# Kernel tuning notes

Measured on AMD Instinct MI355X. Metric: run time of the kernel, lower is better.

Reference implementation:

```python
import math
import jax, jax.numpy as jnp
import numpy as np

B, S, HID = 1, 2048, 2048
NH, QLR, KVLR = 16, 1536, 512
QKD, QKP, VD = 128, 64, 128          # nope dim, rope dim, v dim
IH, ID, TOPK = 4, 128, 512            # indexer heads, indexer head dim, topk
EPS = 1e-6
NEG = -1e9
_MS = 0.1 * 1.0 * math.log(40.0) + 1.0           # mscale adjustment, rope_factor=40
SCALE = _MS * _MS / math.sqrt(QKD + QKP)          # main attention softmax scale
IDX_SCALE = ID ** -0.5                            # indexer softmax scale


def _freqs_cos_sin():
    # seqlen <= original_max_position_embeddings -> plain RoPE freqs (no YaRN branch)
    freqs = 1.0 / (10000.0 ** (jnp.arange(0, QKP, 2, dtype=jnp.float32) / QKP))  # [QKP/2]
    ang = jnp.outer(jnp.arange(S, dtype=jnp.float32), freqs)                      # [S, QKP/2]
    return jnp.cos(ang)[None, :, None, :], jnp.sin(ang)[None, :, None, :]         # [1,S,1,QKP/2]


def _rope_interleaved(x, cos, sin):
    # pairs are (x[..., 2i], x[..., 2i+1])
    x1, x2 = x[..., 0::2], x[..., 1::2]
    yr = x1 * cos - x2 * sin
    yi = x1 * sin + x2 * cos
    return jnp.stack([yr, yi], axis=-1).reshape(x.shape)


def _rope_half(x, cos, sin):
    # interleaved=False: real = first half, imag = second half; output [reals..., imags...]
    d2 = x.shape[-1] // 2
    x1, x2 = x[..., :d2], x[..., d2:]
    return jnp.concatenate([x1 * cos - x2 * sin, x1 * sin + x2 * cos], axis=-1)


def _rmsnorm(x, w):
    return x * jax.lax.rsqrt(jnp.mean(x * x, axis=-1, keepdims=True) + EPS) * w


def _layernorm(x, w, b):
    m = jnp.mean(x, axis=-1, keepdims=True)
    v = jnp.mean((x - m) ** 2, axis=-1, keepdims=True)
    return (x - m) * jax.lax.rsqrt(v + EPS) * w + b


def _indexer(x, qr, cos, sin, mask3, idx_wq_b, idx_wk, idx_kn_w, idx_kn_b, idx_ww):
    # x, qr detached by caller. mask3: [B,S,S]
    q = (qr @ idx_wq_b.T).reshape(B, S, IH, ID)
    q_pe, q_nope = q[..., :QKP], q[..., QKP:]
    q_pe = _rope_half(q_pe, cos, sin)
    q = jnp.concatenate([q_pe, q_nope], axis=-1)                   # [B,S,IH,ID]
    k = _layernorm(x @ idx_wk.T, idx_kn_w, idx_kn_b)               # [B,S,ID]
    k_pe, k_nope = k[..., :QKP], k[..., QKP:]
    k_pe = _rope_half(k_pe[:, :, None, :], cos, sin)[:, :, 0, :]
    k = jnp.concatenate([k_pe, k_nope], axis=-1)                   # [B,S,ID]
    weights = (x @ idx_ww.T) * (IH ** -0.5)                        # [B,S,IH]
    logits = jnp.einsum('bthd,bsd->bths', q, k) * IDX_SCALE        # [B,T,IH,S]
    logits = jax.nn.relu(logits)
    logits = jnp.einsum('bths,bth->bts', logits, weights)          # weighted head sum
    logits = logits + mask3
    topk_vals, topk_idx = jax.lax.top_k(logits, TOPK)
    log_topk_prob = jax.nn.log_softmax(topk_vals, axis=-1)
    return topk_idx, log_topk_prob


def reference(hidden_states, attention_mask, wq_down, q_ln_w, wq_up, wkv_down,
              kv_ln_w, wk_up, wv_up, wo, idx_wq_b, idx_wk, idx_kn_w, idx_kn_b, idx_ww):
    x = jnp.swapaxes(hidden_states, 0, 1)                          # [B,S,HID]
    mask3 = attention_mask[:, 0]                                   # [B,S,S]
    cos, sin = _freqs_cos_sin()

    qr = _rmsnorm(x @ wq_down.T, q_ln_w)                           # [B,S,QLR]
    q = (qr @ wq_up.T).reshape(B, S, NH, QKD + QKP)
    q_nope, q_pe = q[..., :QKD], q[..., QKD:]
    q_pe = _rope_interleaved(q_pe, cos, sin)

    kv = x @ wkv_down.T                                            # [B,S,KVLR+QKP]
    kv_c, k_pe = kv[..., :KVLR], kv[..., KVLR:]
    kv_c = _rmsnorm(kv_c, kv_ln_w)
    k_pe = _rope_interleaved(k_pe[:, :, None, :], cos, sin)        # [B,S,1,QKP]

    k_up_w = wk_up.reshape(NH, QKD, KVLR)
    q_abs = jnp.einsum('bshd,hdc->bshc', q_nope, k_up_w)           # absorbed q
    q_abs = jnp.concatenate([q_abs, q_pe], axis=-1)                # [B,S,NH,KVLR+QKP]

    topk_idx, log_topk_prob = _indexer(
        jax.lax.stop_gradient(x), jax.lax.stop_gradient(qr), cos, sin, mask3,
        idx_wq_b, idx_wk, idx_kn_w, idx_kn_b, idx_ww)

    keys = jnp.concatenate([kv_c, k_pe[:, :, 0, :]], axis=-1)      # [B,T,KVLR+QKP]
    scores = jnp.einsum('bshd,btd->bsht', q_abs, keys) * SCALE     # [B,S,NH,T]
    scores = scores + mask3[:, :, None, :]
    bi = jnp.arange(B)[:, None, None]
    si = jnp.arange(S)[None, :, None]
    index_mask = jnp.full((B, S, S), NEG, jnp.float32).at[bi, si, topk_idx].set(0.0)
    scores = scores + index_mask[:, :, None, :]
    probs = jax.nn.softmax(scores, axis=-1)                        # [B,S,NH,T]
    attn_out = jnp.einsum('bsht,btd->bshd', probs, kv_c)           # values = kv_c

    idx4 = jnp.broadcast_to(topk_idx[:, :, None, :], (B, S, NH, TOPK))
    sparse_probs = jnp.take_along_axis(jax.lax.stop_gradient(probs), idx4, axis=-1)
    attn_score = sparse_probs.sum(axis=2)
    attn_score = attn_score / attn_score.sum(axis=-1, keepdims=True)
    tgt = jnp.clip(jnp.log(attn_score), -100.0, 0.0)
    inp = jnp.clip(log_topk_prob, -100.0, 0.0)
    kl = jnp.sum(jnp.exp(tgt) * (tgt - inp))

    v_up_w = wv_up.reshape(NH, VD, KVLR)
    attn_out = jnp.einsum('bshc,hdc->bshd', attn_out, v_up_w)
    out = attn_out.reshape(B, S, NH * VD) @ wo.T
    return jnp.swapaxes(out, 0, 1), kl


def setup_inputs():
    key = jax.random.key(0)
    ks = jax.random.split(key, 12)
    p = lambda k, sh: jax.random.normal(k, sh, jnp.float32) * 0.02
    hidden_states = jax.random.normal(ks[0], (S, B, HID), jnp.float32)
    causal = jnp.where(jnp.arange(S)[:, None] >= jnp.arange(S)[None, :], 0.0, NEG).astype(jnp.float32)
    attention_mask = jnp.broadcast_to(causal, (B, 1, S, S))
    return dict(
        hidden_states=hidden_states,
        attention_mask=attention_mask,
        wq_down=p(ks[1], (QLR, HID)),
        q_ln_w=jnp.ones((QLR,), jnp.float32),
        wq_up=p(ks[2], (NH * (QKD + QKP), QLR)),
        wkv_down=p(ks[3], (KVLR + QKP, HID)),
        kv_ln_w=jnp.ones((KVLR,), jnp.float32),
        wk_up=p(ks[4], (NH * QKD, KVLR)),
        wv_up=p(ks[5], (NH * VD, KVLR)),
        wo=p(ks[6], (HID, NH * VD)),
        idx_wq_b=p(ks[7], (IH * ID, QLR)),
        idx_wk=p(ks[8], (ID, HID)),
        idx_kn_w=jnp.ones((ID,), jnp.float32),
        idx_kn_b=jnp.zeros((ID,), jnp.float32),
        idx_ww=p(ks[9], (IH, HID)),
    )
```

## Files before the change

kernel.cpp:

```cpp
#include <hip/hip_runtime.h>
#include <hip/hip_bf16.h>
#include <math.h>

typedef __hip_bfloat16 bf16;
typedef __attribute__((ext_vector_type(8))) short short8v;
typedef __attribute__((ext_vector_type(4))) float f32x4;

static constexpr float EPS_   = 1e-6f;
static constexpr float NEG_   = -1000000000.0f;
static constexpr float SCALE_ = 0.13523378f;
static constexpr float IDXSC_ = 0.08838834764832f;
static constexpr double LN10K_32 = 0.28782313662425575;

#define MFMA16(a, b, c) __builtin_amdgcn_mfma_f32_16x16x32_bf16(a, b, c, 0, 0, 0)

__device__ __forceinline__ void gld16(const void* g, void* l) {
  __builtin_amdgcn_global_load_lds(
      (const __attribute__((address_space(1))) void*)g,
      (__attribute__((address_space(3))) void*)l, 16, 0, 0);
}

static __device__ float block_reduce_op(float v, int op) {
  __shared__ float red_s[16];
  int lane = threadIdx.x & 63, wid = threadIdx.x >> 6;
  #pragma unroll
  for (int off = 32; off > 0; off >>= 1) {
    float o = __shfl_down(v, off);
    v = op ? fmaxf(v, o) : (v + o);
  }
  __syncthreads();
  if (lane == 0) red_s[wid] = v;
  __syncthreads();
  if (threadIdx.x == 0) {
    int nw = ((int)blockDim.x + 63) >> 6;
    float r = red_s[0];
    for (int i = 1; i < nw; i++) r = op ? fmaxf(r, red_s[i]) : (r + red_s[i]);
    red_s[0] = r;
  }
  __syncthreads();
  return red_s[0];
}

__global__ __launch_bounds__(256) void f2b_kernel(const float* __restrict__ in,
                                                  bf16* __restrict__ out, long n) {
  long i = ((long)blockIdx.x * 256 + threadIdx.x) * 4;
  if (i + 3 < n) {
    float4 v = *(const float4*)(in + i);
    out[i] = __float2bfloat16(v.x); out[i+1] = __float2bfloat16(v.y);
    out[i+2] = __float2bfloat16(v.z); out[i+3] = __float2bfloat16(v.w);
  } else {
    for (int j = 0; j < 4 && i + j < n; j++) out[i+j] = __float2bfloat16(in[i+j]);
  }
}

template <int BT, int OB>
__global__ __launch_bounds__(256) void gemm_bf16(
    const bf16* __restrict__ A, const bf16* __restrict__ B, void* __restrict__ Cv,
    int M, int N, int K, int lda, int ldb, int ldc, long sA, long sB, long sC) {
  A += (long)blockIdx.z * sA;
  B += (long)blockIdx.z * sB;
  __shared__ bf16 As[4096];
  __shared__ bf16 Bs[4096];
  const int m0 = blockIdx.y * 128, n0 = blockIdx.x * 128;
  const int tid = threadIdx.x;
  const int wave = tid >> 6, lane = tid & 63, g = lane >> 4, li = lane & 15;
  const int mB = (wave >> 1) * 64, nB = (wave & 1) * 64;
  f32x4 acc[4][4];
  #pragma unroll
  for (int i = 0; i < 4; i++)
    #pragma unroll
    for (int j = 0; j < 4; j++) acc[i][j] = (f32x4){0.f, 0.f, 0.f, 0.f};

  for (int k0 = 0; k0 < K; k0 += 32) {
    #pragma unroll
    for (int r2 = 0; r2 < 2; r2++) {
      int idx = r2 * 256 + tid;
      int row = idx >> 2, ko = (idx & 3) * 8;
      gld16(A + (long)(m0 + row) * lda + k0 + ko, &As[idx * 8]);
    }
    if (BT) {
      #pragma unroll
      for (int r2 = 0; r2 < 2; r2++) {
        int idx = r2 * 256 + tid;
        int row = idx >> 2, ko = (idx & 3) * 8;
        int rr = n0 + row; if (rr >= N) rr = N - 1;
        gld16(B + (long)rr * ldb + k0 + ko, &Bs[idx * 8]);
      }
    } else {
      int k = tid >> 3, nb = (tid & 7) * 16;
      const bf16* src = B + (long)(k0 + k) * ldb + n0 + nb;
      short8v v0 = *(const short8v*)src;
      short8v v1 = *(const short8v*)(src + 8);
      #pragma unroll
      for (int j = 0; j < 8; j++) {
        Bs[(nb + j) * 32 + k]     = ((const bf16*)&v0)[j];
        Bs[(nb + 8 + j) * 32 + k] = ((const bf16*)&v1)[j];
      }
    }
    __syncthreads();
    short8v af[4], bfr[4];
    #pragma unroll
    for (int mt = 0; mt < 4; mt++) af[mt]  = *(const short8v*)&As[(mB + mt*16 + li) * 32 + g*8];
    #pragma unroll
    for (int nt = 0; nt < 4; nt++) bfr[nt] = *(const short8v*)&Bs[(nB + nt*16 + li) * 32 + g*8];
    #pragma unroll
    for (int mt = 0; mt < 4; mt++)
      #pragma unroll
      for (int nt = 0; nt < 4; nt++)
        acc[mt][nt] = MFMA16(af[mt], bfr[nt], acc[mt][nt]);
    __syncthreads();
  }
  #pragma unroll
  for (int mt = 0; mt < 4; mt++)
    #pragma unroll
    for (int nt = 0; nt < 4; nt++)
      #pragma unroll
      for (int r = 0; r < 4; r++) {
        int row = m0 + mB + mt*16 + g*4 + r;
        int col = n0 + nB + nt*16 + li;
        if (col < N) {
          long off = (long)blockIdx.z * sC + (long)row * ldc + col;
          if (OB) ((bf16*)Cv)[off] = __float2bfloat16(acc[mt][nt][r]);
          else    ((float*)Cv)[off] = acc[mt][nt][r];
        }
      }
}

__global__ __launch_bounds__(256) void rmsnorm_b_kernel(const float* __restrict__ x,
                                                        const float* __restrict__ w,
                                                        bf16* __restrict__ out, int D) {
  const float* r = x + (long)blockIdx.x * D;
  bf16* o = out + (long)blockIdx.x * D;
  float ss = 0.f;
  for (int i = threadIdx.x; i < D; i += 256) { float v = r[i]; ss = fmaf(v, v, ss); }
  ss = block_reduce_op(ss, 0);
  float sc = rsqrtf(ss / (float)D + EPS_);
  for (int i = threadIdx.x; i < D; i += 256) o[i] = __float2bfloat16(r[i] * sc * w[i]);
}

__global__ __launch_bounds__(256) void kv_norm_rope_kernel(const float* __restrict__ kv,
                                                           const float* __restrict__ w,
                                                           bf16* __restrict__ keys_b) {
  int s = blockIdx.x;
  const float* r = kv + (long)s * 576;
  float ss = 0.f;
  for (int i = threadIdx.x; i < 512; i += 256) { float v = r[i]; ss = fmaf(v, v, ss); }
  ss = block_reduce_op(ss, 0);
  float sc = rsqrtf(ss / 512.f + EPS_);
  for (int i = threadIdx.x; i < 512; i += 256)
    keys_b[(long)s * 576 + i] = __float2bfloat16(r[i] * sc * w[i]);
  if (threadIdx.x < 32) {
    int j = threadIdx.x;
    float f = (float)exp(-(double)j * LN10K_32);
    float ang = (float)s * f;
    float c = cosf(ang), sn = sinf(ang);
    float x1 = r[512 + 2*j], x2 = r[512 + 2*j + 1];
    keys_b[(long)s * 576 + 512 + 2*j]     = __float2bfloat16(x1 * c - x2 * sn);
    keys_b[(long)s * 576 + 512 + 2*j + 1] = __float2bfloat16(x1 * sn + x2 * c);
  }
}

__global__ __launch_bounds__(256) void rope_q_kernel(const bf16* __restrict__ q,
                                                     bf16* __restrict__ qabs) {
  int idx = blockIdx.x * 256 + threadIdx.x;
  int j = idx & 31, h = (idx >> 5) & 15, s = idx >> 9;
  float f = (float)exp(-(double)j * LN10K_32);
  float ang = (float)s * f;
  float c = cosf(ang), sn = sinf(ang);
  const bf16* src = q + (long)s * 3072 + h * 192 + 128;
  float x1 = __bfloat162float(src[2*j]), x2 = __bfloat162float(src[2*j+1]);
  bf16* dst = qabs + (long)s * 9216 + h * 576 + 512;
  dst[2*j]     = __float2bfloat16(x1 * c - x2 * sn);
  dst[2*j + 1] = __float2bfloat16(x1 * sn + x2 * c);
}

__global__ __launch_bounds__(256) void rope_qi_kernel(bf16* __restrict__ qi) {
  int idx = blockIdx.x * 256 + threadIdx.x;
  int j = idx & 31, ih = (idx >> 5) & 3, s = idx >> 7;
  float f = (float)exp(-(double)j * LN10K_32);
  float ang = (float)s * f;
  float c = cosf(ang), sn = sinf(ang);
  bf16* p = qi + (long)s * 512 + ih * 128;
  float x1 = __bfloat162float(p[j]), x2 = __bfloat162float(p[32 + j]);
  p[j]      = __float2bfloat16(x1 * c - x2 * sn);
  p[32 + j] = __float2bfloat16(x1 * sn + x2 * c);
}

__global__ __launch_bounds__(128) void ki_ln_rope_kernel(const float* __restrict__ kt,
                                                         const float* __restrict__ w,
                                                         const float* __restrict__ b,
                                                         bf16* __restrict__ ki_b) {
  int s = blockIdx.x, d = threadIdx.x;
  float v = kt[(long)s * 128 + d];
  float m = block_reduce_op(v, 0) * (1.f / 128.f);
  float dv = v - m;
  float var = block_reduce_op(dv * dv, 0) * (1.f / 128.f);
  float y = dv * rsqrtf(var + EPS_) * w[d] + b[d];
  __shared__ float ys[128];
  ys[d] = y;
  __syncthreads();
  float out;
  if (d < 64) {
    int j = d & 31;
    float f = (float)exp(-(double)j * LN10K_32);
    float ang = (float)s * f;
    float c = cosf(ang), sn = sinf(ang);
    float x1 = ys[j], x2 = ys[32 + j];
    out = (d < 32) ? (x1 * c - x2 * sn) : (x1 * sn + x2 * c);
  } else out = y;
  ki_b[(long)s * 128 + d] = __float2bfloat16(out);
}

__global__ __launch_bounds__(256) void wgt_kernel(const float* __restrict__ x,
                                                  const float* __restrict__ ww,
                                                  float* __restrict__ wgt) {
  int s = blockIdx.x;
  float a0 = 0, a1 = 0, a2 = 0, a3 = 0;
  for (int i = threadIdx.x; i < 2048; i += 256) {
    float xv = x[(long)s * 2048 + i];
    a0 = fmaf(xv, ww[i], a0);
    a1 = fmaf(xv, ww[2048 + i], a1);
    a2 = fmaf(xv, ww[4096 + i], a2);
    a3 = fmaf(xv, ww[6144 + i], a3);
  }
  a0 = block_reduce_op(a0, 0);
  a1 = block_reduce_op(a1, 0);
  a2 = block_reduce_op(a2, 0);
  a3 = block_reduce_op(a3, 0);
  if (threadIdx.x == 0) {
    wgt[s*4+0] = 0.5f*a0; wgt[s*4+1] = 0.5f*a1; wgt[s*4+2] = 0.5f*a2; wgt[s*4+3] = 0.5f*a3;
  }
}

__global__ __launch_bounds__(256) void idx_logits_mfma(const bf16* __restrict__ qi,
                                                       const bf16* __restrict__ ki,
                                                       const float* __restrict__ wgt,
                                                       float* __restrict__ logits) {
  const int t0 = blockIdx.y * 64, s0 = blockIdx.x * 128;
  const int tid = threadIdx.x, wave = tid >> 6, lane = tid & 63;
  const int g = lane >> 4, li = lane & 15;
  if (s0 > t0 + 63) {
    #pragma unroll
    for (int j = 0; j < 8; j++)
      #pragma unroll
      for (int r = 0; r < 4; r++) {
        int t = t0 + wave*16 + g*4 + r, sidx = s0 + j*16 + li;
        logits[(long)t * 2048 + sidx] = NEG_;
      }
    return;
  }
  f32x4 acc[8];
  #pragma unroll
  for (int j = 0; j < 8; j++) acc[j] = (f32x4){0.f,0.f,0.f,0.f};
  #pragma unroll
  for (int h = 0; h < 4; h++) {
    f32x4 tmp[8];
    #pragma unroll
    for (int j = 0; j < 8; j++) tmp[j] = (f32x4){0.f,0.f,0.f,0.f};
    const bf16* arow = qi + ((long)(t0 + wave*16 + li) * 4 + h) * 128 + g*8;
    #pragma unroll
    for (int ks = 0; ks < 4; ks++) {
      short8v a = *(const short8v*)(arow + ks*32);
      #pragma unroll
      for (int j = 0; j < 8; j++) {
        const bf16* brow = ki + (long)(s0 + j*16 + li) * 128 + ks*32 + g*8;
        tmp[j] = MFMA16(a, *(const short8v*)brow, tmp[j]);
      }
    }
    #pragma unroll
    for (int r = 0; r < 4; r++) {
      float wv = wgt[(t0 + wave*16 + g*4 + r)*4 + h];
      #pragma unroll
      for (int j = 0; j < 8; j++)
        acc[j][r] += fmaxf(tmp[j][r] * IDXSC_, 0.f) * wv;
    }
  }
  #pragma unroll
  for (int j = 0; j < 8; j++)
    #pragma unroll
    for (int r = 0; r < 4; r++) {
      int t = t0 + wave*16 + g*4 + r, sidx = s0 + j*16 + li;
      logits[(long)t * 2048 + sidx] = acc[j][r] + (sidx <= t ? 0.f : NEG_);
    }
}

__global__ __launch_bounds__(256) void topk_kernel(const float* __restrict__ logits,
                                                   int* __restrict__ tki,
                                                   float* __restrict__ tkv,
                                                   float* __restrict__ logZ) {
  int t = blockIdx.x;
  __shared__ unsigned skeys[2048];
  __shared__ unsigned hist[256];
  __shared__ float svals[512];
  __shared__ int s_want;
  __shared__ unsigned s_prefix;
  const float* row = logits + (long)t * 2048;
  for (int i = threadIdx.x; i < 2048; i += 256) {
    unsigned u = __float_as_uint(row[i]);
    skeys[i] = (u & 0x80000000u) ? ~u : (u | 0x80000000u);
  }
  if (threadIdx.x == 0) { s_want = 512; s_prefix = 0u; }
  __syncthreads();
  for (int shift = 24; shift >= 0; shift -= 8) {
    if (threadIdx.x < 256) hist[threadIdx.x] = 0u;
    __syncthreads();
    unsigned pmask = (shift == 24) ? 0u : (0xFFFFFFFFu << (shift + 8));
    unsigned pref = s_prefix;
    for (int i = threadIdx.x; i < 2048; i += 256) {
      unsigned k = skeys[i];
      if ((k & pmask) == pref) atomicAdd(&hist[(k >> shift) & 255u], 1u);
    }
    __syncthreads();
    if (threadIdx.x == 0) {
      int want = s_want;
      unsigned cum = 0;
      int b = 255;
      for (;; b--) {
        cum += hist[b];
        if ((int)cum >= want || b == 0) break;
      }
      s_want = want - (int)(cum - hist[b]);
      s_prefix = pref | ((unsigned)b << shift);
    }
    __syncthreads();
  }
  unsigned T = s_prefix;
  int want_eq = s_want;
  int c_gt = 512 - want_eq;
  if (threadIdx.x < 64) {
    int n_gt = 0, n_eq = 0;
    unsigned long long below = (1ull << threadIdx.x) - 1ull;
    for (int base = 0; base < 2048; base += 64) {
      int i = base + (int)threadIdx.x;
      unsigned k = skeys[i];
      bool gt = (k > T), eq = (k == T);
      unsigned long long bg = __ballot(gt);
      unsigned long long be = __ballot(eq);
      int slot = -1;
      if (gt) slot = n_gt + (int)__popcll(bg & below);
      else if (eq) {
        int er = n_eq + (int)__popcll(be & below);
        if (er < want_eq) slot = c_gt + er;
      }
      if (slot >= 0) {
        unsigned bits = (k & 0x80000000u) ? (k ^ 0x80000000u) : ~k;
        float val = __uint_as_float(bits);
        tki[(long)t * 512 + slot] = i;
        tkv[(long)t * 512 + slot] = val;
        svals[slot] = val;
      }
      n_gt += (int)__popcll(bg);
      n_eq += (int)__popcll(be);
    }
  }
  __syncthreads();
  float m = -3.4e38f;
  for (int i = threadIdx.x; i < 512; i += 256) m = fmaxf(m, svals[i]);
  m = block_reduce_op(m, 1);
  float se = 0.f;
  for (int i = threadIdx.x; i < 512; i += 256) se += expf(svals[i] - m);
  se = block_reduce_op(se, 0);
  if (threadIdx.x == 0) logZ[t] = m + logf(se);
}

__global__ __launch_bounds__(256, 6) void attn_qk(
    const bf16* __restrict__ qabs, const bf16* __restrict__ keys,
    const int* __restrict__ tki, const float* __restrict__ tkv,
    const float* __restrict__ logZ, bf16* __restrict__ Pg,
    float* __restrict__ kl) {
  const int s = 2047 - blockIdx.x;
  const int tid = threadIdx.x;
  const int wave = tid >> 6, lane = tid & 63, g = lane >> 4, li = lane & 15;
  __shared__ int idxs[512];
  __shared__ __align__(16) bf16 ph[16 * 512];
  __shared__ float red[64];
  __shared__ float mxf[16], dnf[16];

  for (int i = tid; i < 512; i += 256) idxs[i] = tki[(long)s * 512 + i];
  __syncthreads();

  const bf16* qrow = qabs + (long)s * 9216 + li * 576 + g * 8;
  f32x4 accS[8];
  int kid[8];
  const bf16* kr[8];
  #pragma unroll
  for (int j = 0; j < 8; j++) {
    accS[j] = (f32x4){0.f,0.f,0.f,0.f};
    kid[j] = idxs[(wave * 8 + j) * 16 + li];
    kr[j] = keys + (long)kid[j] * 576 + g * 8;
  }
  short8v af = *(const short8v*)qrow;
  short8v kf[8];
  #pragma unroll
  for (int j = 0; j < 8; j++) kf[j] = *(const short8v*)kr[j];
  for (int ks = 0; ks < 18; ks++) {
    const int nko = (ks < 17 ? ks + 1 : 17) * 32;
    short8v afn = *(const short8v*)(qrow + nko);
    short8v nx[8];
    #pragma unroll
    for (int j = 0; j < 8; j++) nx[j] = *(const short8v*)(kr[j] + nko);
    #pragma unroll
    for (int j = 0; j < 8; j++) accS[j] = MFMA16(af, kf[j], accS[j]);
    af = afn;
    #pragma unroll
    for (int j = 0; j < 8; j++) kf[j] = nx[j];
  }

  float e[8][4];
  float m4[4];
  #pragma unroll
  for (int r = 0; r < 4; r++) m4[r] = -3.4e38f;
  #pragma unroll
  for (int j = 0; j < 8; j++) {
    float mask = (kid[j] <= s) ? 0.f : NEG_;
    #pragma unroll
    for (int r = 0; r < 4; r++) {
      e[j][r] = accS[j][r] * SCALE_ + mask;
      m4[r] = fmaxf(m4[r], e[j][r]);
    }
  }
  #pragma unroll
  for (int d = 1; d < 16; d <<= 1)
    #pragma unroll
    for (int r = 0; r < 4; r++) m4[r] = fmaxf(m4[r], __shfl_xor(m4[r], d));
  if (li == 0)
    #pragma unroll
    for (int r = 0; r < 4; r++) red[wave * 16 + g * 4 + r] = m4[r];
  __syncthreads();
  if (tid < 16) mxf[tid] = fmaxf(fmaxf(red[tid], red[16 + tid]), fmaxf(red[32 + tid], red[48 + tid]));
  __syncthreads();
  float d4[4] = {0.f, 0.f, 0.f, 0.f};
  #pragma unroll
  for (int j = 0; j < 8; j++)
    #pragma unroll
    for (int r = 0; r < 4; r++) {
      e[j][r] = __expf(e[j][r] - mxf[g * 4 + r]);
      d4[r] += e[j][r];
    }
  #pragma unroll
  for (int d = 1; d < 16; d <<= 1)
    #pragma unroll
    for (int r = 0; r < 4; r++) d4[r] += __shfl_xor(d4[r], d);
  if (li == 0)
    #pragma unroll
    for (int r = 0; r < 4; r++) red[wave * 16 + g * 4 + r] = d4[r];
  __syncthreads();
  if (tid < 16) dnf[tid] = red[tid] + red[16 + tid] + red[32 + tid] + red[48 + tid];
  __syncthreads();

  float invd[4];
  #pragma unroll
  for (int r = 0; r < 4; r++) invd[r] = 1.f / dnf[g * 4 + r];

  float tasj[8];
  #pragma unroll
  for (int j = 0; j < 8; j++) {
    float t = 0.f;
    #pragma unroll
    for (int r = 0; r < 4; r++) t += e[j][r] * invd[r];
    t += __shfl_xor(t, 16);
    t += __shfl_xor(t, 32);
    tasj[j] = t;
  }
  float klacc = 0.f;
  if (g == 0) {
    float lz = logZ[s];
    #pragma unroll
    for (int j = 0; j < 8; j++) {
      int slot = (wave * 8 + j) * 16 + li;
      float tgt = fminf(fmaxf(logf(tasj[j] * 0.0625f), -100.f), 0.f);
      float inp = fminf(fmaxf(tkv[(long)s * 512 + slot] - lz, -100.f), 0.f);
      klacc += expf(tgt) * (tgt - inp);
    }
  }
  #pragma unroll
  for (int d = 1; d < 16; d <<= 1) klacc += __shfl_xor(klacc, d);
  if (lane == 0) atomicAdd(kl, klacc);

  const int m = s >> 7;
  const int Km = (m + 1) << 7;
  const int rr = s & 127;
  bf16* Pbase = Pg + 131072L * m * (m + 1);
  for (int base = 0; base < Km; base += 512) {
    const int cw = min(512, Km - base);
    __syncthreads();
    { uint4 z = {0,0,0,0};
      for (int i = tid; i < 1024; i += 256) ((uint4*)ph)[i] = z; }
    __syncthreads();
    #pragma unroll
    for (int j = 0; j < 8; j++) {
      int kk = kid[j] - base;
      if (0 <= kk && kk < 512) {
        #pragma unroll
        for (int r = 0; r < 4; r++)
          ph[(g * 4 + r) * 512 + kk] = __float2bfloat16(e[j][r] * invd[r]);
      }
    }
    __syncthreads();
    for (int u = tid; u < 1024; u += 256) {
      int h = u >> 6, c = (u & 63) * 8;
      if (c < cw)
        *(short8v*)(Pbase + ((long)(h * 128 + rr) * Km + base + c)) =
            *(const short8v*)&ph[h * 512 + c];
    }
  }
}

__global__ __launch_bounds__(256) void attn_pv(const bf16* __restrict__ Pg,
                                               const bf16* __restrict__ keys,
                                               bf16* __restrict__ aoc) {
  const int m = 15 - blockIdx.y;
  const int h = blockIdx.z;
  const int Km = (m + 1) << 7;
  const bf16* A = Pg + 131072L * m * (m + 1) + (long)h * 128 * Km;
  const int n0 = blockIdx.x * 128;
  __shared__ bf16 As[4096];
  __shared__ bf16 Bs[4096];
  const int tid = threadIdx.x;
  const int wave = tid >> 6, lane = tid & 63, g = lane >> 4, li = lane & 15;
  const int mB = (wave >> 1) * 64, nB = (wave & 1) * 64;
  f32x4 acc[4][4];
  #pragma unroll
  for (int i = 0; i < 4; i++)
    #pragma unroll
    for (int j = 0; j < 4; j++) acc[i][j] = (f32x4){0.f, 0.f, 0.f, 0.f};

  for (int k0 = 0; k0 < Km; k0 += 32) {
    #pragma unroll
    for (int r2 = 0; r2 < 2; r2++) {
      int idx = r2 * 256 + tid;
      int row = idx >> 2, ko = (idx & 3) * 8;
      gld16(A + (long)row * Km + k0 + ko, &As[idx * 8]);
    }
    {
      int k = tid >> 3, nb = (tid & 7) * 16;
      const bf16* src = keys + (long)(k0 + k) * 576 + n0 + nb;
      short8v v0 = *(const short8v*)src;
      short8v v1 = *(const short8v*)(src + 8);
      #pragma unroll
      for (int j = 0; j < 8; j++) {
        Bs[(nb + j) * 32 + k]     = ((const bf16*)&v0)[j];
        Bs[(nb + 8 + j) * 32 + k] = ((const bf16*)&v1)[j];
      }
    }
    __syncthreads();
    short8v af[4], bfr[4];
    #pragma unroll
    for (int mt = 0; mt < 4; mt++) af[mt]  = *(const short8v*)&As[(mB + mt*16 + li) * 32 + g*8];
    #pragma unroll
    for (int nt = 0; nt < 4; nt++) bfr[nt] = *(const short8v*)&Bs[(nB + nt*16 + li) * 32 + g*8];
    #pragma unroll
    for (int mt = 0; mt < 4; mt++)
      #pragma unroll
      for (int nt = 0; nt < 4; nt++)
        acc[mt][nt] = MFMA16(af[mt], bfr[nt], acc[mt][nt]);
    __syncthreads();
  }
  #pragma unroll
  for (int mt = 0; mt < 4; mt++)
    #pragma unroll
    for (int nt = 0; nt < 4; nt++)
      #pragma unroll
      for (int r = 0; r < 4; r++) {
        int row = m * 128 + mB + mt*16 + g*4 + r;
        int col = n0 + nB + nt*16 + li;
        aoc[(long)row * 8192 + h * 512 + col] = __float2bfloat16(acc[mt][nt][r]);
      }
}

__global__ void zero_kernel(float* p) {
  if (threadIdx.x == 0 && blockIdx.x == 0) p[0] = 0.f;
}
__global__ void copykl_kernel(const float* src, float* dst) { dst[0] = src[0]; }

extern "C" void kernel_launch(void* const* d_in, const int* in_sizes, int n_in,
                              void* d_out, int out_size, void* d_ws, size_t ws_size,
                              hipStream_t stream) {
  (void)in_sizes; (void)n_in; (void)out_size; (void)ws_size;
  const float* x        = (const float*)d_in[0];
  const float* wq_down  = (const float*)d_in[2];
  const float* q_ln_w   = (const float*)d_in[3];
  const float* wq_up    = (const float*)d_in[4];
  const float* wkv_down = (const float*)d_in[5];
  const float* kv_ln_w  = (const float*)d_in[6];
  const float* wk_up    = (const float*)d_in[7];
  const float* wv_up    = (const float*)d_in[8];
  const float* wo       = (const float*)d_in[9];
  const float* idx_wq_b = (const float*)d_in[10];
  const float* idx_wk   = (const float*)d_in[11];
  const float* idx_kn_w = (const float*)d_in[12];
  const float* idx_kn_b = (const float*)d_in[13];
  const float* idx_ww   = (const float*)d_in[14];
  float* out = (float*)d_out;

  char* w = (char*)d_ws;
  size_t off = 0;
  auto alloc = [&](size_t bytes) { void* p = w + off; off += (bytes + 255) & ~255ul; return p; };
  bf16* keys_b  = (bf16*)alloc(2048L*576*2);
  bf16* qabs_b  = (bf16*)alloc(2048L*9216*2);
  bf16* aoc_b   = (bf16*)alloc(2048L*8192*2);
  bf16* ao_b    = (bf16*)alloc(2048L*2048*2);
  bf16* wvu_b   = (bf16*)alloc(16L*128*512*2);
  bf16* wo_b    = (bf16*)alloc(2048L*2048*2);
  float* tkv    = (float*)alloc(2048L*512*4);
  float* logZ   = (float*)alloc(2048*4);
  float* klbuf  = (float*)alloc(64);
  int*   tki    = (int*)alloc(2048L*512*4);
  size_t scratch0 = off;
  bf16* Pg = (bf16*)(w + scratch0);
  float* qr     = (float*)alloc(2048L*1536*4);
  float* kvtmp  = (float*)alloc(2048L*576*4);
  float* kitmp  = (float*)alloc(2048L*128*4);
  float* logits = (float*)alloc(2048L*2048*4);
  float* wgt    = (float*)alloc(2048L*4*4);
  bf16* x_b     = (bf16*)alloc(2048L*2048*2);
  bf16* qr_b    = (bf16*)alloc(2048L*1536*2);
  bf16* q_b     = (bf16*)alloc(2048L*3072*2);
  bf16* qi_b    = (bf16*)alloc(2048L*512*2);
  bf16* ki_b    = (bf16*)alloc(2048L*128*2);
  bf16* wqd_b   = (bf16*)alloc(1536L*2048*2);
  bf16* wqu_b   = (bf16*)alloc(3072L*1536*2);
  bf16* wkv_b   = (bf16*)alloc(576L*2048*2);
  bf16* wku_b   = (bf16*)alloc(16L*128*512*2);
  bf16* iwq_b   = (bf16*)alloc(512L*1536*2);
  bf16* iwk_b   = (bf16*)alloc(128L*2048*2);
  size_t pg_end = scratch0 + 131072ul*16*17*2;
  if (off < pg_end) off = pg_end;

  dim3 b256(256);
  auto cvt = [&](const float* src, bf16* dst, long n) {
    f2b_kernel<<<(int)((n + 1023) / 1024), b256, 0, stream>>>(src, dst, n);
  };
  cvt(x, x_b, 2048L*2048);
  cvt(wq_down, wqd_b, 1536L*2048);
  cvt(wq_up, wqu_b, 3072L*1536);
  cvt(wkv_down, wkv_b, 576L*2048);
  cvt(wk_up, wku_b, 16L*128*512);
  cvt(wv_up, wvu_b, 16L*128*512);
  cvt(wo, wo_b, 2048L*2048);
  cvt(idx_wq_b, iwq_b, 512L*1536);
  cvt(idx_wk, iwk_b, 128L*2048);

  gemm_bf16<1,0><<<dim3(12,16), b256, 0, stream>>>(x_b, wqd_b, qr, 2048,1536,2048, 2048,2048,1536, 0,0,0);
  rmsnorm_b_kernel<<<2048, b256, 0, stream>>>(qr, q_ln_w, qr_b, 1536);
  gemm_bf16<1,1><<<dim3(24,16), b256, 0, stream>>>(qr_b, wqu_b, q_b, 2048,3072,1536, 1536,1536,3072, 0,0,0);
  gemm_bf16<1,0><<<dim3(5,16), b256, 0, stream>>>(x_b, wkv_b, kvtmp, 2048,576,2048, 2048,2048,576, 0,0,0);
  kv_norm_rope_kernel<<<2048, b256, 0, stream>>>(kvtmp, kv_ln_w, keys_b);
  rope_q_kernel<<<4096, b256, 0, stream>>>(q_b, qabs_b);
  gemm_bf16<0,1><<<dim3(4,16,16), b256, 0, stream>>>(q_b, wku_b, qabs_b, 2048,512,128, 3072,512,9216, 192, 128L*512, 576);
  gemm_bf16<1,1><<<dim3(4,16), b256, 0, stream>>>(qr_b, iwq_b, qi_b, 2048,512,1536, 1536,1536,512, 0,0,0);
  rope_qi_kernel<<<1024, b256, 0, stream>>>(qi_b);
  gemm_bf16<1,0><<<dim3(1,16), b256, 0, stream>>>(x_b, iwk_b, kitmp, 2048,128,2048, 2048,2048,128, 0,0,0);
  ki_ln_rope_kernel<<<2048, dim3(128), 0, stream>>>(kitmp, idx_kn_w, idx_kn_b, ki_b);
  wgt_kernel<<<2048, b256, 0, stream>>>(x, idx_ww, wgt);
  idx_logits_mfma<<<dim3(16,32), b256, 0, stream>>>(qi_b, ki_b, wgt, logits);
  topk_kernel<<<2048, b256, 0, stream>>>(logits, tki, tkv, logZ);
  zero_kernel<<<1, 64, 0, stream>>>(klbuf);
  attn_qk<<<2048, b256, 0, stream>>>(qabs_b, keys_b, tki, tkv, logZ, Pg, klbuf);
  attn_pv<<<dim3(4,16,16), b256, 0, stream>>>(Pg, keys_b, aoc_b);
  gemm_bf16<1,1><<<dim3(1,16,16), b256, 0, stream>>>(aoc_b, wvu_b, ao_b, 2048,128,512, 8192,512,2048, 512, 128L*512, 128);
  gemm_bf16<1,0><<<dim3(16,16), b256, 0, stream>>>(ao_b, wo_b, out, 2048,2048,2048, 2048,2048,2048, 0,0,0);
  copykl_kernel<<<1, 1, 0, stream>>>(klbuf, out + 4194304L);
}
```

Measured before the change: 1.005 ms.

## Parallelize topk bucket scan and deepen attn_qk gather prefetch

The serial single-thread bucket search in topk_kernel is replaced by a parallel suffix-sum scan over the 256-bin histogram, so every thread helps find the threshold bucket. In attn_qk, the gathered key and query fragment loads are double-buffered two k-steps ahead with a fully unrolled loop, and the occupancy hint is lowered from 6 to 4 blocks to make room for the extra registers. The scan adds many __syncthreads per radix pass, and lower occupancy may cut latency hiding elsewhere.

```diff
diff --git a/kernel.cpp b/kernel.cpp
--- a/kernel.cpp
+++ b/kernel.cpp
@@ -289,49 +289,57 @@
                                                    float* __restrict__ tkv,
                                                    float* __restrict__ logZ) {
   int t = blockIdx.x;
+  const int tid = threadIdx.x;
   __shared__ unsigned skeys[2048];
   __shared__ unsigned hist[256];
+  __shared__ unsigned suf[256];
   __shared__ float svals[512];
   __shared__ int s_want;
   __shared__ unsigned s_prefix;
   const float* row = logits + (long)t * 2048;
-  for (int i = threadIdx.x; i < 2048; i += 256) {
+  for (int i = tid; i < 2048; i += 256) {
     unsigned u = __float_as_uint(row[i]);
     skeys[i] = (u & 0x80000000u) ? ~u : (u | 0x80000000u);
   }
-  if (threadIdx.x == 0) { s_want = 512; s_prefix = 0u; }
+  if (tid == 0) { s_want = 512; s_prefix = 0u; }
   __syncthreads();
   for (int shift = 24; shift >= 0; shift -= 8) {
-    if (threadIdx.x < 256) hist[threadIdx.x] = 0u;
+    hist[tid] = 0u;
     __syncthreads();
     unsigned pmask = (shift == 24) ? 0u : (0xFFFFFFFFu << (shift + 8));
     unsigned pref = s_prefix;
-    for (int i = threadIdx.x; i < 2048; i += 256) {
+    int want = s_want;
+    for (int i = tid; i < 2048; i += 256) {
       unsigned k = skeys[i];
       if ((k & pmask) == pref) atomicAdd(&hist[(k >> shift) & 255u], 1u);
     }
     __syncthreads();
-    if (threadIdx.x == 0) {
-      int want = s_want;
-      unsigned cum = 0;
-      int b = 255;
-      for (;; b--) {
-        cum += hist[b];
-        if ((int)cum >= want || b == 0) break;
-      }
-      s_want = want - (int)(cum - hist[b]);
-      s_prefix = pref | ((unsigned)b << shift);
+    suf[tid] = hist[tid];
+    __syncthreads();
+    #pragma unroll
+    for (int d = 1; d < 256; d <<= 1) {
+      unsigned v = suf[tid];
+      unsigned add = (tid + d < 256) ? suf[tid + d] : 0u;
+      __syncthreads();
+      suf[tid] = v + add;
+      __syncthreads();
+    }
+    unsigned Sb = suf[tid];
+    unsigned Sb1 = (tid < 255) ? suf[tid + 1] : 0u;
+    if ((int)Sb >= want && (int)Sb1 < want) {
+      s_want = want - (int)Sb1;
+      s_prefix = pref | ((unsigned)tid << shift);
     }
     __syncthreads();
   }
   unsigned T = s_prefix;
   int want_eq = s_want;
   int c_gt = 512 - want_eq;
-  if (threadIdx.x < 64) {
+  if (tid < 64) {
     int n_gt = 0, n_eq = 0;
-    unsigned long long below = (1ull << threadIdx.x) - 1ull;
+    unsigned long long below = (1ull << tid) - 1ull;
     for (int base = 0; base < 2048; base += 64) {
-      int i = base + (int)threadIdx.x;
+      int i = base + (int)tid;
       unsigned k = skeys[i];
       bool gt = (k > T), eq = (k == T);
       unsigned long long bg = __ballot(gt);
@@ -355,15 +363,15 @@
   }
   __syncthreads();
   float m = -3.4e38f;
-  for (int i = threadIdx.x; i < 512; i += 256) m = fmaxf(m, svals[i]);
+  for (int i = tid; i < 512; i += 256) m = fmaxf(m, svals[i]);
   m = block_reduce_op(m, 1);
   float se = 0.f;
-  for (int i = threadIdx.x; i < 512; i += 256) se += expf(svals[i] - m);
+  for (int i = tid; i < 512; i += 256) se += expf(svals[i] - m);
   se = block_reduce_op(se, 0);
-  if (threadIdx.x == 0) logZ[t] = m + logf(se);
-}
-
-__global__ __launch_bounds__(256, 6) void attn_qk(
+  if (tid == 0) logZ[t] = m + logf(se);
+}
+
+__global__ __launch_bounds__(256, 4) void attn_qk(
     const bf16* __restrict__ qabs, const bf16* __restrict__ keys,
     const int* __restrict__ tki, const float* __restrict__ tkv,
     const float* __restrict__ logZ, bf16* __restrict__ Pg,
@@ -389,21 +397,27 @@
     kid[j] = idxs[(wave * 8 + j) * 16 + li];
     kr[j] = keys + (long)kid[j] * 576 + g * 8;
   }
-  short8v af = *(const short8v*)qrow;
-  short8v kf[8];
-  #pragma unroll
-  for (int j = 0; j < 8; j++) kf[j] = *(const short8v*)kr[j];
+  short8v afv[2];
+  short8v kfv[2][8];
+  afv[0] = *(const short8v*)qrow;
+  afv[1] = *(const short8v*)(qrow + 32);
+  #pragma unroll
+  for (int j = 0; j < 8; j++) kfv[0][j] = *(const short8v*)kr[j];
+  #pragma unroll
+  for (int j = 0; j < 8; j++) kfv[1][j] = *(const short8v*)(kr[j] + 32);
+  #pragma unroll
   for (int ks = 0; ks < 18; ks++) {
-    const int nko = (ks < 17 ? ks + 1 : 17) * 32;
-    short8v afn = *(const short8v*)(qrow + nko);
+    const int cur = ks & 1;
+    const int nko = (ks + 2 < 18 ? ks + 2 : 17) * 32;
+    short8v anx = *(const short8v*)(qrow + nko);
     short8v nx[8];
     #pragma unroll
     for (int j = 0; j < 8; j++) nx[j] = *(const short8v*)(kr[j] + nko);
     #pragma unroll
-    for (int j = 0; j < 8; j++) accS[j] = MFMA16(af, kf[j], accS[j]);
-    af = afn;
-    #pragma unroll
-    for (int j = 0; j < 8; j++) kf[j] = nx[j];
+    for (int j = 0; j < 8; j++) accS[j] = MFMA16(afv[cur], kfv[cur][j], accS[j]);
+    afv[cur] = anx;
+    #pragma unroll
+    for (int j = 0; j < 8; j++) kfv[cur][j] = nx[j];
   }
 
   float e[8][4];
```

After: 945.8 us. -5.9%, faster.
